# Kernel tuning notes

Measured on AMD Instinct MI355X. Metric: run time of the kernel, lower is better.

Reference implementation:

```python
import jax, jax.numpy as jnp
import numpy as np

V = 1_000_000   # number of nodes in graph (embedding table rows)
D_IN = 128      # input feature dim
D_OUT = 384     # output dim (3 * D_OUT//3)
N_UNIQ = 20_000 # unique nodes in batch
K = 32          # neighbors per node (num_walks)
B = 40_000      # batch of node lookups


def setup_inputs() -> dict:
    key = jax.random.key(0)
    ks = jax.random.split(key, 12)
    d3 = D_OUT // 3
    return {
        "unique_nodes": jax.random.randint(ks[0], (N_UNIQ,), 0, V),
        "adj_neighbors": jax.random.randint(ks[1], (N_UNIQ, K), 0, V),
        "dis_neighbors": jax.random.randint(ks[2], (N_UNIQ, K), 0, V),
        "nodes_idx": jax.random.randint(ks[3], (B,), 0, N_UNIQ),
        "feat_table": jax.random.normal(ks[4], (V, D_IN), dtype=jnp.float32),
        # linear weights stored [in, out] (transposed vs torch nn.Linear)
        "W_self": jax.random.uniform(ks[5], (D_IN, d3), minval=-0.1, maxval=0.1, dtype=jnp.float32),
        "W_adj": jax.random.uniform(ks[6], (D_IN, d3), minval=-0.1, maxval=0.1, dtype=jnp.float32),
        "W_dis": jax.random.uniform(ks[7], (D_IN, d3), minval=-0.1, maxval=0.1, dtype=jnp.float32),
        "bias": jnp.zeros((D_OUT,), dtype=jnp.float32),
        "WC_w": jax.random.normal(ks[8], (D_OUT, D_OUT), dtype=jnp.float32) * 0.05,
        "WC_b": jnp.zeros((D_OUT,), dtype=jnp.float32),
    }


def reference(unique_nodes, adj_neighbors, dis_neighbors, nodes_idx,
              feat_table, W_self, W_adj, W_dis, bias, WC_w, WC_b):
    # MeanAggregator: one-hot mask.mm(embed) == mean of gathered neighbor feats
    adj_agg = jnp.mean(feat_table[adj_neighbors], axis=1)   # [N,K,D] -> [N,D]
    dis_agg = jnp.mean(feat_table[dis_neighbors], axis=1)
    self_feats = feat_table[unique_nodes] @ W_self           # [N, D_OUT/3]
    adj_feats = adj_agg @ W_adj
    dis_feats = dis_agg @ W_dis
    # concat + bias, WC linear, leakyReLU(0.2), L2-normalize (eval mode: no dropout)
    feats = jnp.concatenate([self_feats, adj_feats, dis_feats], axis=-1) + bias
    feats = feats @ WC_w + WC_b
    feats = jnp.where(feats >= 0, feats, 0.2 * feats)
    norm = jnp.maximum(jnp.linalg.norm(feats, axis=-1, keepdims=True), 1e-12)
    feats = feats / norm
    return feats[nodes_idx]  # [B, D_OUT]
```

## Files before the change

kernel.cpp:

```cpp
#include <hip/hip_runtime.h>
#include <hip/hip_bf16.h>

#define N_UNIQ 20000
#define K_NBR 32
#define BATCH 40000

typedef unsigned short ushort_t;
typedef __bf16 bfrag __attribute__((ext_vector_type(8)));
typedef float  ffrag __attribute__((ext_vector_type(4)));

__device__ __forceinline__ ushort_t f2bf(float f) {
    unsigned u = __builtin_bit_cast(unsigned, f);
    unsigned r = u + 0x7fffu + ((u >> 16) & 1u);
    return (ushort_t)(r >> 16);
}
__device__ __forceinline__ unsigned pack2(float x, float y) {
    return (unsigned)f2bf(x) | ((unsigned)f2bf(y) << 16);
}

__global__ void pack_kernel(const float* __restrict__ Ws,
                            const float* __restrict__ Wa,
                            const float* __restrict__ Wd,
                            const float* __restrict__ WC,
                            uint4* __restrict__ wp1, uint4* __restrict__ wp2) {
    int t = blockIdx.x * blockDim.x + threadIdx.x;
    int l = t & 63, q = l >> 4, m = l & 15;
    ushort_t v[8];
    if (t < 6144) {
        int g   = t >> 11;
        int rem = t & 2047;
        int nt  = rem >> 8;
        int kk  = (rem >> 6) & 3;
        const float* W = (g == 0) ? Ws : ((g == 1) ? Wa : Wd);
#pragma unroll
        for (int j = 0; j < 8; j++)
            v[j] = f2bf(W[(kk * 32 + q * 8 + j) * 128 + nt * 16 + m]);
        uint4 u; __builtin_memcpy(&u, v, 16);
        wp1[t] = u;
    } else {
        int t2 = t - 6144;
        int nt = t2 / 768;
        int kk = (t2 >> 6) % 12;
#pragma unroll
        for (int j = 0; j < 8; j++)
            v[j] = f2bf(WC[(kk * 32 + q * 8 + j) * 384 + nt * 16 + m]);
        uint4 u; __builtin_memcpy(&u, v, 16);
        wp2[t2] = u;
    }
}

__global__ void agg_kernel(const int* __restrict__ uniq,
                           const int* __restrict__ adjn,
                           const int* __restrict__ disn,
                           const float* __restrict__ feat,
                           ushort_t* __restrict__ F) {
    int wave = (blockIdx.x * blockDim.x + threadIdx.x) >> 6;
    int l = threadIdx.x & 63;
    if (wave >= N_UNIQ) return;

    int my = (l < 32) ? adjn[wave * K_NBR + l] : disn[wave * K_NBR + (l - 32)];

    float a0 = 0.f, a1 = 0.f, d0 = 0.f, d1 = 0.f;
#pragma unroll 8
    for (int i = 0; i < 32; i++) {
        int ra = __shfl(my, i);
        int rd = __shfl(my, 32 + i);
        float2 fa = *(const float2*)(feat + (size_t)ra * 128 + l * 2);
        float2 fd = *(const float2*)(feat + (size_t)rd * 128 + l * 2);
        a0 += fa.x; a1 += fa.y;
        d0 += fd.x; d1 += fd.y;
    }
    float2 fs = *(const float2*)(feat + (size_t)uniq[wave] * 128 + l * 2);

    const float inv = 1.0f / 32.0f;
    ushort_t* row = F + (size_t)wave * 384;
    *(unsigned*)(row + l * 2)       = pack2(fs.x, fs.y);
    *(unsigned*)(row + 128 + l * 2) = pack2(a0 * inv, a1 * inv);
    *(unsigned*)(row + 256 + l * 2) = pack2(d0 * inv, d1 * inv);
}

__global__ void gemm1_kernel(ushort_t* __restrict__ F,
                             const uint4* __restrict__ wp1,
                             const float* __restrict__ bias) {
    int wv = blockIdx.x * 4 + (threadIdx.x >> 6);
    if (wv >= N_UNIQ / 16) return;
    int l = threadIdx.x & 63, q = l >> 4, m = l & 15;
    int m0 = wv * 16;

    uint4 a[12];
    const ushort_t* xrow = F + (size_t)(m0 + m) * 384;
#pragma unroll
    for (int kk = 0; kk < 12; kk++)
        a[kk] = *(const uint4*)(xrow + kk * 32 + q * 8);

    ushort_t outv[24][4];
#pragma unroll
    for (int nt = 0; nt < 24; nt++) {
        int g = nt >> 3;
        ffrag acc = {0.f, 0.f, 0.f, 0.f};
        const uint4* wp = wp1 + (size_t)nt * 4 * 64;
#pragma unroll
        for (int kk = 0; kk < 4; kk++) {
            bfrag bf = __builtin_bit_cast(bfrag, wp[kk * 64 + l]);
            bfrag af = __builtin_bit_cast(bfrag, a[g * 4 + kk]);
            acc = __builtin_amdgcn_mfma_f32_16x16x32_bf16(af, bf, acc, 0, 0, 0);
        }
        float bv = bias[nt * 16 + m];
#pragma unroll
        for (int r = 0; r < 4; r++) outv[nt][r] = f2bf(acc[r] + bv);
    }
#pragma unroll
    for (int nt = 0; nt < 24; nt++) {
        int col = nt * 16 + m;
#pragma unroll
        for (int r = 0; r < 4; r++)
            F[(size_t)(m0 + q * 4 + r) * 384 + col] = outv[nt][r];
    }
}

__global__ void gemm2_kernel(const ushort_t* __restrict__ F,
                             const uint4* __restrict__ wp2,
                             const float* __restrict__ wcb,
                             float* __restrict__ G) {
    int wv = blockIdx.x * 4 + (threadIdx.x >> 6);
    if (wv >= N_UNIQ / 16) return;
    int l = threadIdx.x & 63, q = l >> 4, m = l & 15;
    int m0 = wv * 16;

    uint4 a[12];
    const ushort_t* xrow = F + (size_t)(m0 + m) * 384;
#pragma unroll
    for (int kk = 0; kk < 12; kk++)
        a[kk] = *(const uint4*)(xrow + kk * 32 + q * 8);

    float vals[24][4];
    float ss[4] = {0.f, 0.f, 0.f, 0.f};
#pragma unroll
    for (int nt = 0; nt < 24; nt++) {
        ffrag acc = {0.f, 0.f, 0.f, 0.f};
        const uint4* wp = wp2 + (size_t)nt * 12 * 64;
#pragma unroll
        for (int kk = 0; kk < 12; kk++) {
            bfrag bf = __builtin_bit_cast(bfrag, wp[kk * 64 + l]);
            bfrag af = __builtin_bit_cast(bfrag, a[kk]);
            acc = __builtin_amdgcn_mfma_f32_16x16x32_bf16(af, bf, acc, 0, 0, 0);
        }
        float bv = wcb[nt * 16 + m];
#pragma unroll
        for (int r = 0; r < 4; r++) {
            float v = acc[r] + bv;
            v = (v >= 0.f) ? v : 0.2f * v;
            vals[nt][r] = v;
            ss[r] += v * v;
        }
    }
#pragma unroll
    for (int r = 0; r < 4; r++) {
        float s = ss[r];
        s += __shfl_xor(s, 1);
        s += __shfl_xor(s, 2);
        s += __shfl_xor(s, 4);
        s += __shfl_xor(s, 8);
        float nrm = fmaxf(sqrtf(s), 1e-12f);
        ss[r] = 1.0f / nrm;
    }
#pragma unroll
    for (int nt = 0; nt < 24; nt++) {
        int col = nt * 16 + m;
#pragma unroll
        for (int r = 0; r < 4; r++)
            G[(size_t)(m0 + q * 4 + r) * 384 + col] = vals[nt][r] * ss[r];
    }
}

__global__ void gather_kernel(const int* __restrict__ nidx,
                              const uint4* __restrict__ G4,
                              uint4* __restrict__ out4) {
    int t = blockIdx.x * blockDim.x + threadIdx.x;
    if (t >= BATCH * 96) return;
    int b = t / 96, c = t - b * 96;
    int row = nidx[b];
    out4[(size_t)b * 96 + c] = G4[(size_t)row * 96 + c];
}

extern "C" void kernel_launch(void* const* d_in, const int* in_sizes, int n_in,
                              void* d_out, int out_size, void* d_ws, size_t ws_size,
                              hipStream_t stream) {
    const int*   uniq = (const int*)d_in[0];
    const int*   adjn = (const int*)d_in[1];
    const int*   disn = (const int*)d_in[2];
    const int*   nidx = (const int*)d_in[3];
    const float* feat = (const float*)d_in[4];
    const float* Ws   = (const float*)d_in[5];
    const float* Wa   = (const float*)d_in[6];
    const float* Wd   = (const float*)d_in[7];
    const float* bias = (const float*)d_in[8];
    const float* WC   = (const float*)d_in[9];
    const float* wcb  = (const float*)d_in[10];

    ushort_t* F   = (ushort_t*)d_ws;
    float*    G   = (float*)((char*)d_ws + 15360000);
    uint4*    wp1 = (uint4*)((char*)d_ws + 46080000);
    uint4*    wp2 = (uint4*)((char*)d_ws + 46178304);

    pack_kernel<<<96, 256, 0, stream>>>(Ws, Wa, Wd, WC, wp1, wp2);
    agg_kernel<<<N_UNIQ / 4, 256, 0, stream>>>(uniq, adjn, disn, feat, F);
    gemm1_kernel<<<(N_UNIQ / 16 + 3) / 4, 256, 0, stream>>>(F, wp1, bias);
    gemm2_kernel<<<(N_UNIQ / 16 + 3) / 4, 256, 0, stream>>>(F, wp2, wcb, G);
    gather_kernel<<<BATCH * 96 / 256, 256, 0, stream>>>(nidx, (const uint4*)G, (uint4*)d_out);
}
```

Before: 812.7 us.

## Fuse weight packing into aggregation, split wave halves across adj/dis with float4 loads

Merges the weight-pack kernel into the aggregation kernel as extra leading blocks, removing one launch. The aggregation now assigns the first half-wave to adjacency neighbors and the second to distance neighbors. Each lane loads a float4, so one 512-byte row is fetched per half-wave and neighbor indices are read as scalar loads instead of shuffles. The final gather uses nontemporal stores to avoid polluting cache with output. Risk: only half the lanes do the self-feature load, and the fused blocks may slightly imbalance scheduling.

Result: no change. 813.3 us (+0.1%).

```diff
diff --git a/kernel.cpp b/kernel.cpp
--- a/kernel.cpp
+++ b/kernel.cpp
@@ -8,6 +8,7 @@
 typedef unsigned short ushort_t;
 typedef __bf16 bfrag __attribute__((ext_vector_type(8)));
 typedef float  ffrag __attribute__((ext_vector_type(4)));
+typedef unsigned uvec4 __attribute__((ext_vector_type(4)));
 
 __device__ __forceinline__ ushort_t f2bf(float f) {
     unsigned u = __builtin_bit_cast(unsigned, f);
@@ -18,65 +19,84 @@
     return (unsigned)f2bf(x) | ((unsigned)f2bf(y) << 16);
 }
 
-__global__ void pack_kernel(const float* __restrict__ Ws,
-                            const float* __restrict__ Wa,
-                            const float* __restrict__ Wd,
-                            const float* __restrict__ WC,
-                            uint4* __restrict__ wp1, uint4* __restrict__ wp2) {
-    int t = blockIdx.x * blockDim.x + threadIdx.x;
-    int l = t & 63, q = l >> 4, m = l & 15;
-    ushort_t v[8];
-    if (t < 6144) {
-        int g   = t >> 11;
-        int rem = t & 2047;
-        int nt  = rem >> 8;
-        int kk  = (rem >> 6) & 3;
-        const float* W = (g == 0) ? Ws : ((g == 1) ? Wa : Wd);
-#pragma unroll
-        for (int j = 0; j < 8; j++)
-            v[j] = f2bf(W[(kk * 32 + q * 8 + j) * 128 + nt * 16 + m]);
-        uint4 u; __builtin_memcpy(&u, v, 16);
-        wp1[t] = u;
-    } else {
-        int t2 = t - 6144;
-        int nt = t2 / 768;
-        int kk = (t2 >> 6) % 12;
-#pragma unroll
-        for (int j = 0; j < 8; j++)
-            v[j] = f2bf(WC[(kk * 32 + q * 8 + j) * 384 + nt * 16 + m]);
-        uint4 u; __builtin_memcpy(&u, v, 16);
-        wp2[t2] = u;
-    }
-}
-
-__global__ void agg_kernel(const int* __restrict__ uniq,
-                           const int* __restrict__ adjn,
-                           const int* __restrict__ disn,
-                           const float* __restrict__ feat,
-                           ushort_t* __restrict__ F) {
-    int wave = (blockIdx.x * blockDim.x + threadIdx.x) >> 6;
-    int l = threadIdx.x & 63;
-    if (wave >= N_UNIQ) return;
-
-    int my = (l < 32) ? adjn[wave * K_NBR + l] : disn[wave * K_NBR + (l - 32)];
-
-    float a0 = 0.f, a1 = 0.f, d0 = 0.f, d1 = 0.f;
-#pragma unroll 8
-    for (int i = 0; i < 32; i++) {
-        int ra = __shfl(my, i);
-        int rd = __shfl(my, 32 + i);
-        float2 fa = *(const float2*)(feat + (size_t)ra * 128 + l * 2);
-        float2 fd = *(const float2*)(feat + (size_t)rd * 128 + l * 2);
-        a0 += fa.x; a1 += fa.y;
-        d0 += fd.x; d1 += fd.y;
-    }
-    float2 fs = *(const float2*)(feat + (size_t)uniq[wave] * 128 + l * 2);
+__global__ void pack_agg_kernel(const float* __restrict__ Ws,
+                                const float* __restrict__ Wa,
+                                const float* __restrict__ Wd,
+                                const float* __restrict__ WC,
+                                uint4* __restrict__ wp1,
+                                uint4* __restrict__ wp2,
+                                const int* __restrict__ uniq,
+                                const int* __restrict__ adjn,
+                                const int* __restrict__ disn,
+                                const float* __restrict__ feat,
+                                ushort_t* __restrict__ F) {
+    if (blockIdx.x < 96) {
+        int t = blockIdx.x * blockDim.x + threadIdx.x;
+        int l = t & 63, q = l >> 4, m = l & 15;
+        ushort_t v[8];
+        if (t < 6144) {
+            int g   = t >> 11;
+            int rem = t & 2047;
+            int nt  = rem >> 8;
+            int kk  = (rem >> 6) & 3;
+            const float* W = (g == 0) ? Ws : ((g == 1) ? Wa : Wd);
+#pragma unroll
+            for (int j = 0; j < 8; j++)
+                v[j] = f2bf(W[(kk * 32 + q * 8 + j) * 128 + nt * 16 + m]);
+            uint4 u; __builtin_memcpy(&u, v, 16);
+            wp1[t] = u;
+        } else {
+            int t2 = t - 6144;
+            int nt = t2 / 768;
+            int kk = (t2 >> 6) % 12;
+#pragma unroll
+            for (int j = 0; j < 8; j++)
+                v[j] = f2bf(WC[(kk * 32 + q * 8 + j) * 384 + nt * 16 + m]);
+            uint4 u; __builtin_memcpy(&u, v, 16);
+            wp2[t2] = u;
+        }
+        return;
+    }
+
+    int node = ((blockIdx.x - 96) << 2) + (threadIdx.x >> 6);
+    node = __builtin_amdgcn_readfirstlane(node);
+    if (node >= N_UNIQ) return;
+
+    const int l   = threadIdx.x & 63;
+    const int lm  = l & 31;
+    const bool isdis = (l >= 32);
+
+    const int* __restrict__ na = adjn + node * K_NBR;
+    const int* __restrict__ nd = disn + node * K_NBR;
+    const float4* __restrict__ feat4 = (const float4*)feat;
+
+    float ax = 0.f, ay = 0.f, az = 0.f, aw = 0.f;
+#pragma unroll
+    for (int i = 0; i < K_NBR; i++) {
+        int ra = na[i];
+        int rd = nd[i];
+        int r  = isdis ? rd : ra;
+        int idx = r * 32 + lm;
+        float4 v = feat4[idx];
+        ax += v.x; ay += v.y; az += v.z; aw += v.w;
+    }
 
     const float inv = 1.0f / 32.0f;
-    ushort_t* row = F + (size_t)wave * 384;
-    *(unsigned*)(row + l * 2)       = pack2(fs.x, fs.y);
-    *(unsigned*)(row + 128 + l * 2) = pack2(a0 * inv, a1 * inv);
-    *(unsigned*)(row + 256 + l * 2) = pack2(d0 * inv, d1 * inv);
+    ushort_t* row = F + (size_t)node * 384;
+
+    uint2 mpk;
+    mpk.x = pack2(ax * inv, ay * inv);
+    mpk.y = pack2(az * inv, aw * inv);
+    *(uint2*)(row + 128 + (isdis ? 128 : 0) + lm * 4) = mpk;
+
+    if (!isdis) {
+        int rs = uniq[node];
+        float4 sv = feat4[rs * 32 + lm];
+        uint2 spk;
+        spk.x = pack2(sv.x, sv.y);
+        spk.y = pack2(sv.z, sv.w);
+        *(uint2*)(row + lm * 4) = spk;
+    }
 }
 
 __global__ void gemm1_kernel(ushort_t* __restrict__ F,
@@ -174,13 +194,14 @@
 }
 
 __global__ void gather_kernel(const int* __restrict__ nidx,
-                              const uint4* __restrict__ G4,
-                              uint4* __restrict__ out4) {
+                              const uvec4* __restrict__ G4,
+                              uvec4* __restrict__ out4) {
     int t = blockIdx.x * blockDim.x + threadIdx.x;
     if (t >= BATCH * 96) return;
     int b = t / 96, c = t - b * 96;
     int row = nidx[b];
-    out4[(size_t)b * 96 + c] = G4[(size_t)row * 96 + c];
+    uvec4 v = G4[(size_t)row * 96 + c];
+    __builtin_nontemporal_store(v, &out4[(size_t)b * 96 + c]);
 }
 
 extern "C" void kernel_launch(void* const* d_in, const int* in_sizes, int n_in,
@@ -203,9 +224,9 @@
     uint4*    wp1 = (uint4*)((char*)d_ws + 46080000);
     uint4*    wp2 = (uint4*)((char*)d_ws + 46178304);
 
-    pack_kernel<<<96, 256, 0, stream>>>(Ws, Wa, Wd, WC, wp1, wp2);
-    agg_kernel<<<N_UNIQ / 4, 256, 0, stream>>>(uniq, adjn, disn, feat, F);
+    pack_agg_kernel<<<96 + N_UNIQ / 4, 256, 0, stream>>>(
+        Ws, Wa, Wd, WC, wp1, wp2, uniq, adjn, disn, feat, F);
     gemm1_kernel<<<(N_UNIQ / 16 + 3) / 4, 256, 0, stream>>>(F, wp1, bias);
     gemm2_kernel<<<(N_UNIQ / 16 + 3) / 4, 256, 0, stream>>>(F, wp2, wcb, G);
-    gather_kernel<<<BATCH * 96 / 256, 256, 0, stream>>>(nidx, (const uint4*)G, (uint4*)d_out);
-}
+    gather_kernel<<<BATCH * 96 / 256, 256, 0, stream>>>(nidx, (const uvec4*)G, (uvec4*)d_out);
+}
```
